# Optimization experiments

Hardware: AMD Instinct MI355X
Metric: run time of the kernel (lower is better)

The kernel has to match this reference:

```python
import jax, jax.numpy as jnp
import numpy as np

N, E = 100000, 1600000
IN_C, OUT_C, H, EDGE_DIM = 128, 64, 2, 4
NEG_SLOPE = 0.2
LN_EPS = 1e-5


def setup_inputs() -> dict:
    key = jax.random.key(0)
    ks = jax.random.split(key, 12)
    s = 1.0 / np.sqrt(IN_C)
    inp = {
        "x": jax.random.normal(ks[0], (N, IN_C), jnp.float32),
        "edge_index": jax.random.randint(ks[1], (2, E), 0, N, jnp.int64),
        "edge_attr": jax.random.normal(ks[2], (E, EDGE_DIM), jnp.float32),
        "W": jax.random.normal(ks[3], (IN_C, H * OUT_C), jnp.float32) * s,
        "att_src": jax.random.normal(ks[4], (H, OUT_C), jnp.float32) * s,
        "att_dst": jax.random.normal(ks[5], (H, OUT_C), jnp.float32) * s,
        "W_edge": jax.random.normal(ks[6], (EDGE_DIM, H * OUT_C), jnp.float32) * 0.5,
        "att_edge": jax.random.normal(ks[7], (H, OUT_C), jnp.float32) * s,
        "bias": jnp.zeros((OUT_C,), jnp.float32),
        "gamma": jnp.ones((OUT_C,), jnp.float32),
        "beta": jnp.zeros((OUT_C,), jnp.float32),
    }
    return inp


def reference(x, edge_index, edge_attr, W, att_src, att_dst, W_edge, att_edge, bias, gamma, beta):
    n = x.shape[0]
    src, dst = edge_index[0], edge_index[1]
    # shared src/dst linear (PyG GATConv with single input tensor)
    h = (x @ W).reshape(n, H, OUT_C)                       # [N,H,C]
    a_src = jnp.einsum("nhc,hc->nh", h, att_src)          # [N,H]
    a_dst = jnp.einsum("nhc,hc->nh", h, att_dst)          # [N,H]
    e = (edge_attr @ W_edge).reshape(-1, H, OUT_C)         # [E,H,C]
    a_edge = jnp.einsum("ehc,hc->eh", e, att_edge)        # [E,H]
    alpha = jax.nn.leaky_relu(a_src[src] + a_dst[dst] + a_edge, NEG_SLOPE)  # [E,H]
    # segment softmax over edges grouped by destination node
    amax = jax.ops.segment_max(alpha, dst, num_segments=n)
    ex = jnp.exp(alpha - amax[dst])
    denom = jax.ops.segment_sum(ex, dst, num_segments=n)
    w = ex / (denom[dst] + 1e-16)                          # [E,H]
    msg = h[src] * w[:, :, None]                           # [E,H,C]
    out = jax.ops.segment_sum(msg, dst, num_segments=n)    # [N,H,C]
    out = out.mean(axis=1) + bias                          # concat=False -> head mean
    # LayerNorm + ReLU
    mu = out.mean(-1, keepdims=True)
    var = ((out - mu) ** 2).mean(-1, keepdims=True)
    out = (out - mu) * jax.lax.rsqrt(var + LN_EPS) * gamma + beta
    return jax.nn.relu(out)
```

## Files before the change

### kernel.cpp

```cpp
#include <hip/hip_runtime.h>
#include <hip/hip_fp16.h>
#include <math.h>

#define IN_C 128
#define HC   128
#define OUT_C 64
#define NEG_SLOPE 0.2f
#define LN_EPS 1e-5f
#define CHUNK 4096
#define NBMAX 1024

typedef __attribute__((ext_vector_type(8))) short bf16x8;
typedef __attribute__((ext_vector_type(4))) float f32x4;

__device__ inline unsigned bf16pack(float a, float b) {
    unsigned ua = __float_as_uint(a), ub = __float_as_uint(b);
    ua = (ua + 0x7fffu + ((ua >> 16) & 1u)) >> 16;
    ub = (ub + 0x7fffu + ((ub >> 16) & 1u)) >> 16;
    return ua | (ub << 16);
}

__global__ __launch_bounds__(256) void k_pre(const float* __restrict__ W,
                                             const float* __restrict__ W_edge,
                                             const float* __restrict__ att_edge,
                                             const int* __restrict__ ei_dst,
                                             unsigned short* __restrict__ WbfT,
                                             float* __restrict__ V,
                                             int* __restrict__ off,
                                             int E, int NB, int PB) {
    __shared__ int hist[NBMAX];
    int b = blockIdx.x, t = threadIdx.x;
    if (b < 8) {
        #pragma unroll
        for (int i = 0; i < 8; ++i) {
            int idx = b * 2048 + i * 256 + t;
            int k = idx >> 7, col = idx & 127;
            unsigned u = __float_as_uint(W[idx]);
            WbfT[col * 128 + k] =
                (unsigned short)((u + 0x7fffu + ((u >> 16) & 1u)) >> 16);
        }
        return;
    }
    if (b == 8) {
        if (t < 8) {
            int d = t >> 1, h = t & 1;
            float s = 0.f;
            for (int c = 0; c < 64; ++c)
                s += W_edge[d * HC + h * 64 + c] * att_edge[h * 64 + c];
            V[d * 2 + h] = s;
        }
        return;
    }
    int pb = b - 9;
    for (int i = t; i < NB; i += 256) hist[i] = 0;
    __syncthreads();
    int base = pb * CHUNK;
    int lim = E - base; if (lim > CHUNK) lim = CHUNK;
    for (int i = t; i < lim; i += 256)
        atomicAdd(&hist[ei_dst[base + i] >> 7], 1);
    __syncthreads();
    for (int i = t; i < NB; i += 256)
        off[(size_t)i * PB + pb] = hist[i];
}

__global__ __launch_bounds__(256) void k_mid(const float* __restrict__ x,
                                             const unsigned short* __restrict__ WbfT,
                                             const float* __restrict__ attS,
                                             const float* __restrict__ attD,
                                             unsigned* __restrict__ hb,
                                             float* __restrict__ a_src,
                                             float* __restrict__ a_dst, int M,
                                             int* __restrict__ off,
                                             int* __restrict__ bsum,
                                             int nS, int GB) {
    __shared__ unsigned xb[64 * 64];
    const int t = threadIdx.x;
    const int bid = blockIdx.x;

    if (bid >= GB) {
        int* sm = (int*)xb;
        int blk = bid - GB;
        int base = blk * 1024 + t * 4;
        int v0 = 0, v1 = 0, v2 = 0, v3 = 0;
        if (base + 0 < nS) v0 = off[base + 0];
        if (base + 1 < nS) v1 = off[base + 1];
        if (base + 2 < nS) v2 = off[base + 2];
        if (base + 3 < nS) v3 = off[base + 3];
        int s = v0 + v1 + v2 + v3;
        sm[t] = s;
        __syncthreads();
        for (int o = 1; o < 256; o <<= 1) {
            int u = (t >= o) ? sm[t - o] : 0;
            __syncthreads();
            sm[t] += u;
            __syncthreads();
        }
        int excl = sm[t] - s;
        if (base + 0 < nS) off[base + 0] = excl;
        if (base + 1 < nS) off[base + 1] = excl + v0;
        if (base + 2 < nS) off[base + 2] = excl + v0 + v1;
        if (base + 3 < nS) off[base + 3] = excl + v0 + v1 + v2;
        if (t == 255) bsum[blk] = sm[255];
        return;
    }

    const int brow = bid * 64;
    const float4* x4 = (const float4*)x;
    #pragma unroll
    for (int i = 0; i < 8; ++i) {
        int idx = i * 256 + t;
        int row = idx >> 5, c4 = idx & 31;
        float4 v = make_float4(0.f, 0.f, 0.f, 0.f);
        if (brow + row < M) v = x4[(size_t)(brow + row) * 32 + c4];
        unsigned lo = bf16pack(v.x, v.y), hi = bf16pack(v.z, v.w);
        int byte = row * 256 + ((c4 * 8) ^ ((row & 7) << 4));
        *(uint2*)((char*)xb + byte) = make_uint2(lo, hi);
    }
    __syncthreads();

    const int w = t >> 6, lane = t & 63;
    const int col = lane & 15, qr = lane >> 4;
    f32x4 acc[8];
    #pragma unroll
    for (int ct = 0; ct < 8; ++ct) acc[ct] = (f32x4){0.f, 0.f, 0.f, 0.f};

    const int arow = w * 16 + col;
    #pragma unroll
    for (int ks = 0; ks < 4; ++ks) {
        int abyte = arow * 256 + ((ks * 64 + qr * 16) ^ ((arow & 7) << 4));
        bf16x8 af = *(const bf16x8*)((const char*)xb + abyte);
        #pragma unroll
        for (int ct = 0; ct < 8; ++ct) {
            bf16x8 bfr = *(const bf16x8*)&WbfT[(size_t)(ct * 16 + col) * 128 + ks * 32 + qr * 8];
            acc[ct] = __builtin_amdgcn_mfma_f32_16x16x32_bf16(af, bfr, acc[ct], 0, 0, 0);
        }
    }

    float pS0[4], pS1[4], pD0[4], pD1[4];
    #pragma unroll
    for (int r = 0; r < 4; ++r) { pS0[r] = pS1[r] = pD0[r] = pD1[r] = 0.f; }
    #pragma unroll
    for (int ct = 0; ct < 8; ++ct) {
        float s = attS[ct * 16 + col], d = attD[ct * 16 + col];
        #pragma unroll
        for (int r = 0; r < 4; ++r) {
            float a = acc[ct][r];
            if (ct < 4) { pS0[r] += a * s; pD0[r] += a * d; }
            else        { pS1[r] += a * s; pD1[r] += a * d; }
        }
    }
    #pragma unroll
    for (int m = 1; m < 16; m <<= 1) {
        #pragma unroll
        for (int r = 0; r < 4; ++r) {
            pS0[r] += __shfl_xor(pS0[r], m);
            pS1[r] += __shfl_xor(pS1[r], m);
            pD0[r] += __shfl_xor(pD0[r], m);
            pD1[r] += __shfl_xor(pD1[r], m);
        }
    }
    #pragma unroll
    for (int r = 0; r < 4; ++r) {
        int grow = brow + w * 16 + qr * 4 + r;
        if (grow < M) {
            if (col == 0) {
                a_src[2 * grow + 0] = pS0[r];
                a_src[2 * grow + 1] = pS1[r];
                a_dst[2 * grow + 0] = pD0[r];
                a_dst[2 * grow + 1] = pD1[r];
            }
            #pragma unroll
            for (int ct = 0; ct < 4; ++ct)
                hb[(size_t)grow * 64 + ct * 16 + col] =
                    bf16pack(acc[ct][r], acc[ct + 4][r]);
        }
    }
}

__global__ __launch_bounds__(256) void k_part(const int* __restrict__ ei,
                                              const float* __restrict__ ea,
                                              const float* __restrict__ V,
                                              const int* __restrict__ off,
                                              const int* __restrict__ bsum,
                                              uint2* __restrict__ pA,
                                              int E, int NB, int PB, int nb2) {
    __shared__ int cur[NBMAX];
    __shared__ int bs[512];
    int pb = blockIdx.x, t = threadIdx.x;

    int r0 = (t < nb2) ? bsum[t] : 0;
    int r1 = (t + 256 < nb2) ? bsum[t + 256] : 0;
    bs[t] = r0; bs[t + 256] = r1;
    __syncthreads();
    for (int o = 1; o < 512; o <<= 1) {
        int u0 = (t >= o) ? bs[t - o] : 0;
        int u1 = (t + 256 >= o) ? bs[t + 256 - o] : 0;
        __syncthreads();
        bs[t] += u0; bs[t + 256] += u1;
        __syncthreads();
    }
    bs[t] -= r0; bs[t + 256] -= r1;
    __syncthreads();

    for (int i = t; i < NB; i += 256) {
        size_t oi = (size_t)i * PB + pb;
        cur[i] = off[oi] + bs[(int)(oi >> 10)];
    }
    __syncthreads();
    float v0 = V[0], v1 = V[1], v2 = V[2], v3 = V[3];
    float v4 = V[4], v5 = V[5], v6 = V[6], v7 = V[7];
    int base = pb * CHUNK;
    int lim = E - base; if (lim > CHUNK) lim = CHUNK;
    for (int i = t; i < lim; i += 256) {
        int e = base + i;
        int s = ei[e], d = ei[E + e];
        float4 a = ((const float4*)ea)[e];
        float ae0 = a.x * v0 + a.y * v2 + a.z * v4 + a.w * v6;
        float ae1 = a.x * v1 + a.y * v3 + a.z * v5 + a.w * v7;
        int slot = atomicAdd(&cur[d >> 7], 1);
        __half2 h = __floats2half2_rn(ae0, ae1);
        pA[slot] = make_uint2((unsigned)s | ((unsigned)(d & 127) << 17),
                              *reinterpret_cast<unsigned*>(&h));
    }
}

__global__ __launch_bounds__(256) void k_csr(const uint2* __restrict__ pA,
                                             const int* __restrict__ off,
                                             const int* __restrict__ bsum,
                                             const float* __restrict__ a_src,
                                             const float* __restrict__ a_dst,
                                             int* __restrict__ rowptr,
                                             uint2* __restrict__ payload,
                                             int M, int E, int NB, int PB, int nb2) {
    __shared__ int bs[512];
    __shared__ int cnt[128];
    __shared__ int sc[128];
    __shared__ int cur[128];
    __shared__ float2 adl[128];
    int b = blockIdx.x, t = threadIdx.x;
    int n0 = b << 7;
    int nloc = M - n0; if (nloc > 128) nloc = 128;

    int r0 = (t < nb2) ? bsum[t] : 0;
    int r1 = (t + 256 < nb2) ? bsum[t + 256] : 0;
    bs[t] = r0; bs[t + 256] = r1;
    __syncthreads();
    for (int o = 1; o < 512; o <<= 1) {
        int u0 = (t >= o) ? bs[t - o] : 0;
        int u1 = (t + 256 >= o) ? bs[t + 256 - o] : 0;
        __syncthreads();
        bs[t] += u0; bs[t + 256] += u1;
        __syncthreads();
    }
    bs[t] -= r0; bs[t + 256] -= r1;
    if (t < 128) cnt[t] = 0;
    if (t < 128 && t < nloc) adl[t] = ((const float2*)a_dst)[n0 + t];
    __syncthreads();

    size_t o0 = (size_t)b * PB;
    int s0 = off[o0] + bs[(int)(o0 >> 10)];
    int s1 = E;
    if (b + 1 < NB) {
        size_t o1 = (size_t)(b + 1) * PB;
        s1 = off[o1] + bs[(int)(o1 >> 10)];
    }

    for (int i = s0 + t; i < s1; i += 256)
        atomicAdd(&cnt[(pA[i].x >> 17) & 127], 1);
    __syncthreads();
    if (t < 128) sc[t] = cnt[t];
    __syncthreads();
    for (int o = 1; o < 128; o <<= 1) {
        int u = 0;
        if (t < 128 && t >= o) u = sc[t - o];
        __syncthreads();
        if (t < 128) sc[t] += u;
        __syncthreads();
    }
    if (t < 128) {
        int base = s0 + sc[t] - cnt[t];
        cur[t] = base;
        if (t < nloc) rowptr[n0 + t] = base;
    }
    if (b == NB - 1 && t == 0) rowptr[M] = E;
    __syncthreads();
    for (int i = s0 + t; i < s1; i += 256) {
        uint2 p = pA[i];
        int src = p.x & 0x1FFFF;
        int dl = (p.x >> 17) & 127;
        __half2 aeh = *reinterpret_cast<__half2*>(&p.y);
        float ae0 = __low2float(aeh), ae1 = __high2float(aeh);
        float2 as = ((const float2*)a_src)[src];
        float2 ad = adl[dl];
        float al0 = as.x + ad.x + ae0; al0 = al0 > 0.f ? al0 : NEG_SLOPE * al0;
        float al1 = as.y + ad.y + ae1; al1 = al1 > 0.f ? al1 : NEG_SLOPE * al1;
        __half2 hx = __floats2half2_rn(__expf(al0), __expf(al1));
        int pos = atomicAdd(&cur[dl], 1);
        payload[pos] = make_uint2((unsigned)src, *reinterpret_cast<unsigned*>(&hx));
    }
}

__global__ __launch_bounds__(256) void k_gather(const uint2* __restrict__ payload,
                                                const int* __restrict__ rowptr,
                                                const unsigned* __restrict__ hb,
                                                const float* __restrict__ bias,
                                                const float* __restrict__ gamma,
                                                const float* __restrict__ beta,
                                                float* __restrict__ out, int M) {
    __shared__ uint2 stg[4][64];
    int w = threadIdx.x >> 6, lane = threadIdx.x & 63;
    int n = blockIdx.x * 4 + w;
    if (n >= M) return;
    int beg = rowptr[n], end = rowptr[n + 1];
    float acc0 = 0.f, acc1 = 0.f, pe0 = 0.f, pe1 = 0.f;

    for (int base = beg; base < end; base += 64) {
        int cnt = end - base; if (cnt > 64) cnt = 64;
        uint2 p = make_uint2(0u, 0u);
        if (lane < cnt) p = payload[base + lane];
        stg[w][lane] = p;
        {
            __half2 he = *reinterpret_cast<__half2*>(&p.y);
            pe0 += __low2float(he);
            pe1 += __high2float(he);
        }
        int j = 0;
        for (; j + 4 <= cnt; j += 4) {
            uint2 q0 = stg[w][j + 0], q1 = stg[w][j + 1];
            uint2 q2 = stg[w][j + 2], q3 = stg[w][j + 3];
            int s0 = __builtin_amdgcn_readfirstlane((int)q0.x);
            int s1 = __builtin_amdgcn_readfirstlane((int)q1.x);
            int s2 = __builtin_amdgcn_readfirstlane((int)q2.x);
            int s3 = __builtin_amdgcn_readfirstlane((int)q3.x);
            unsigned h0 = (hb + (size_t)s0 * 64)[lane];
            unsigned h1 = (hb + (size_t)s1 * 64)[lane];
            unsigned h2 = (hb + (size_t)s2 * 64)[lane];
            unsigned h3 = (hb + (size_t)s3 * 64)[lane];
            __half2 e0 = *reinterpret_cast<__half2*>(&q0.y);
            __half2 e1 = *reinterpret_cast<__half2*>(&q1.y);
            __half2 e2 = *reinterpret_cast<__half2*>(&q2.y);
            __half2 e3 = *reinterpret_cast<__half2*>(&q3.y);
            acc0 += __low2float(e0)  * __uint_as_float(h0 << 16);
            acc1 += __high2float(e0) * __uint_as_float(h0 & 0xffff0000u);
            acc0 += __low2float(e1)  * __uint_as_float(h1 << 16);
            acc1 += __high2float(e1) * __uint_as_float(h1 & 0xffff0000u);
            acc0 += __low2float(e2)  * __uint_as_float(h2 << 16);
            acc1 += __high2float(e2) * __uint_as_float(h2 & 0xffff0000u);
            acc0 += __low2float(e3)  * __uint_as_float(h3 << 16);
            acc1 += __high2float(e3) * __uint_as_float(h3 & 0xffff0000u);
        }
        for (; j < cnt; ++j) {
            uint2 q0 = stg[w][j];
            int s0 = __builtin_amdgcn_readfirstlane((int)q0.x);
            unsigned h0 = (hb + (size_t)s0 * 64)[lane];
            __half2 e0 = *reinterpret_cast<__half2*>(&q0.y);
            acc0 += __low2float(e0)  * __uint_as_float(h0 << 16);
            acc1 += __high2float(e0) * __uint_as_float(h0 & 0xffff0000u);
        }
    }

    float d0 = pe0, d1 = pe1;
    #pragma unroll
    for (int m = 32; m; m >>= 1) {
        d0 += __shfl_xor(d0, m);
        d1 += __shfl_xor(d1, m);
    }

    float o = 0.5f * (acc0 / (d0 + 1e-16f) + acc1 / (d1 + 1e-16f)) + bias[lane];
    float mu = o;
    #pragma unroll
    for (int m = 32; m; m >>= 1) mu += __shfl_xor(mu, m);
    mu *= (1.f / 64.f);
    float c = o - mu;
    float v = c * c;
    #pragma unroll
    for (int m = 32; m; m >>= 1) v += __shfl_xor(v, m);
    v *= (1.f / 64.f);
    float y = c * rsqrtf(v + LN_EPS) * gamma[lane] + beta[lane];
    out[(size_t)n * OUT_C + lane] = fmaxf(y, 0.f);
}

extern "C" void kernel_launch(void* const* d_in, const int* in_sizes, int n_in,
                              void* d_out, int out_size, void* d_ws, size_t ws_size,
                              hipStream_t stream) {
    const float* x     = (const float*)d_in[0];
    const int*   ei    = (const int*)d_in[1];
    const float* ea    = (const float*)d_in[2];
    const float* W     = (const float*)d_in[3];
    const float* attS  = (const float*)d_in[4];
    const float* attD  = (const float*)d_in[5];
    const float* We    = (const float*)d_in[6];
    const float* attE  = (const float*)d_in[7];
    const float* bias  = (const float*)d_in[8];
    const float* gamma = (const float*)d_in[9];
    const float* beta  = (const float*)d_in[10];

    const int M  = in_sizes[0] / IN_C;
    const int E  = in_sizes[1] / 2;
    const int NB = (M + 127) >> 7;
    const int PB = (E + CHUNK - 1) / CHUNK;
    const int nS = NB * PB;
    const int nb2 = (nS + 1023) / 1024;
    const int GB = (M + 63) / 64;

    char* ws = (char*)d_ws;
    size_t woff = 0;
    auto alloc = [&](size_t bytes) -> void* {
        void* p = ws + woff;
        woff += (bytes + 255) & ~(size_t)255;
        return p;
    };
    unsigned*       hb     = (unsigned*)      alloc((size_t)M * 64 * 4);
    float*          a_src  = (float*)         alloc((size_t)M * 2 * 4);
    float*          a_dst  = (float*)         alloc((size_t)M * 2 * 4);
    int*            off    = (int*)           alloc((size_t)nS * 4);
    int*            bsum   = (int*)           alloc((size_t)nb2 * 4);
    int*            rowptr = (int*)           alloc((size_t)(M + 1) * 4);
    uint2*          pA     = (uint2*)         alloc((size_t)E * 8);
    uint2*          payload= (uint2*)         alloc((size_t)E * 8);
    unsigned short* WbfT   = (unsigned short*)alloc(128 * 128 * 2);
    float*          V      = (float*)         alloc(32);

    k_pre<<<9 + PB, 256, 0, stream>>>(W, We, attE, ei + E, WbfT, V, off, E, NB, PB);
    k_mid<<<GB + nb2, 256, 0, stream>>>(x, WbfT, attS, attD, hb, a_src, a_dst, M,
                                        off, bsum, nS, GB);
    k_part<<<PB, 256, 0, stream>>>(ei, ea, V, off, bsum, pA, E, NB, PB, nb2);
    k_csr<<<NB, 256, 0, stream>>>(pA, off, bsum, a_src, a_dst, rowptr, payload,
                                  M, E, NB, PB, nb2);
    k_gather<<<(M + 3) / 4, 256, 0, stream>>>(payload, rowptr, hb, bias, gamma, beta,
                                              (float*)d_out, M);
}
```

Measured before the change: 164.4 us.

## Move attention exp into partition kernel and share the block-sum scan

Computes the leaky-ReLU attention logits and their exponentials during edge partitioning instead of in the CSR build. The CSR kernel then only counts and scatters payloads, with no random a_src reads. The partition kernel publishes the scanned block sums once, so the CSR kernel no longer repeats that scan. It also doubles the edge chunk size, vectorizes the histogram loads and adds an 8-way unrolled gather loop. The larger chunk halves the number of partition blocks, which may leave parts of the GPU idle in that phase.

```diff
diff --git a/kernel.cpp b/kernel.cpp
--- a/kernel.cpp
+++ b/kernel.cpp
@@ -7,7 +7,7 @@
 #define OUT_C 64
 #define NEG_SLOPE 0.2f
 #define LN_EPS 1e-5f
-#define CHUNK 4096
+#define CHUNK 8192
 #define NBMAX 1024
 
 typedef __attribute__((ext_vector_type(8))) short bf16x8;
@@ -56,8 +56,19 @@
     __syncthreads();
     int base = pb * CHUNK;
     int lim = E - base; if (lim > CHUNK) lim = CHUNK;
-    for (int i = t; i < lim; i += 256)
-        atomicAdd(&hist[ei_dst[base + i] >> 7], 1);
+    for (int i4 = t; i4 * 4 < lim; i4 += 256) {
+        int idx = base + i4 * 4;
+        if (idx + 3 < base + lim) {
+            int4 v = *(const int4*)&ei_dst[idx];
+            atomicAdd(&hist[v.x >> 7], 1);
+            atomicAdd(&hist[v.y >> 7], 1);
+            atomicAdd(&hist[v.z >> 7], 1);
+            atomicAdd(&hist[v.w >> 7], 1);
+        } else {
+            for (int k = idx; k < base + lim; ++k)
+                atomicAdd(&hist[ei_dst[k] >> 7], 1);
+        }
+    }
     __syncthreads();
     for (int i = t; i < NB; i += 256)
         off[(size_t)i * PB + pb] = hist[i];
@@ -180,27 +191,29 @@
 __global__ __launch_bounds__(256) void k_part(const int* __restrict__ ei,
                                               const float* __restrict__ ea,
                                               const float* __restrict__ V,
+                                              const float* __restrict__ a_src,
+                                              const float* __restrict__ a_dst,
                                               const int* __restrict__ off,
                                               const int* __restrict__ bsum,
+                                              int* __restrict__ bsum2,
                                               uint2* __restrict__ pA,
                                               int E, int NB, int PB, int nb2) {
     __shared__ int cur[NBMAX];
-    __shared__ int bs[512];
+    __shared__ int bs[256];
     int pb = blockIdx.x, t = threadIdx.x;
 
     int r0 = (t < nb2) ? bsum[t] : 0;
-    int r1 = (t + 256 < nb2) ? bsum[t + 256] : 0;
-    bs[t] = r0; bs[t + 256] = r1;
-    __syncthreads();
-    for (int o = 1; o < 512; o <<= 1) {
-        int u0 = (t >= o) ? bs[t - o] : 0;
-        int u1 = (t + 256 >= o) ? bs[t + 256 - o] : 0;
+    bs[t] = r0;
+    __syncthreads();
+    for (int o = 1; o < 256; o <<= 1) {
+        int u = (t >= o) ? bs[t - o] : 0;
         __syncthreads();
-        bs[t] += u0; bs[t + 256] += u1;
+        bs[t] += u;
         __syncthreads();
     }
-    bs[t] -= r0; bs[t + 256] -= r1;
-    __syncthreads();
+    bs[t] -= r0;
+    __syncthreads();
+    if (pb == 0 && t < nb2) bsum2[t] = bs[t];
 
     for (int i = t; i < NB; i += 256) {
         size_t oi = (size_t)i * PB + pb;
@@ -211,59 +224,46 @@
     float v4 = V[4], v5 = V[5], v6 = V[6], v7 = V[7];
     int base = pb * CHUNK;
     int lim = E - base; if (lim > CHUNK) lim = CHUNK;
+    #pragma unroll 2
     for (int i = t; i < lim; i += 256) {
         int e = base + i;
         int s = ei[e], d = ei[E + e];
         float4 a = ((const float4*)ea)[e];
         float ae0 = a.x * v0 + a.y * v2 + a.z * v4 + a.w * v6;
         float ae1 = a.x * v1 + a.y * v3 + a.z * v5 + a.w * v7;
+        float2 as = ((const float2*)a_src)[s];
+        float2 ad = ((const float2*)a_dst)[d];
+        float al0 = as.x + ad.x + ae0; al0 = al0 > 0.f ? al0 : NEG_SLOPE * al0;
+        float al1 = as.y + ad.y + ae1; al1 = al1 > 0.f ? al1 : NEG_SLOPE * al1;
+        __half2 hx = __floats2half2_rn(__expf(al0), __expf(al1));
         int slot = atomicAdd(&cur[d >> 7], 1);
-        __half2 h = __floats2half2_rn(ae0, ae1);
         pA[slot] = make_uint2((unsigned)s | ((unsigned)(d & 127) << 17),
-                              *reinterpret_cast<unsigned*>(&h));
+                              *reinterpret_cast<unsigned*>(&hx));
     }
 }
 
 __global__ __launch_bounds__(256) void k_csr(const uint2* __restrict__ pA,
                                              const int* __restrict__ off,
-                                             const int* __restrict__ bsum,
-                                             const float* __restrict__ a_src,
-                                             const float* __restrict__ a_dst,
+                                             const int* __restrict__ bsum2,
                                              int* __restrict__ rowptr,
                                              uint2* __restrict__ payload,
-                                             int M, int E, int NB, int PB, int nb2) {
-    __shared__ int bs[512];
+                                             int M, int E, int NB, int PB) {
     __shared__ int cnt[128];
     __shared__ int sc[128];
     __shared__ int cur[128];
-    __shared__ float2 adl[128];
     int b = blockIdx.x, t = threadIdx.x;
     int n0 = b << 7;
     int nloc = M - n0; if (nloc > 128) nloc = 128;
 
-    int r0 = (t < nb2) ? bsum[t] : 0;
-    int r1 = (t + 256 < nb2) ? bsum[t + 256] : 0;
-    bs[t] = r0; bs[t + 256] = r1;
-    __syncthreads();
-    for (int o = 1; o < 512; o <<= 1) {
-        int u0 = (t >= o) ? bs[t - o] : 0;
-        int u1 = (t + 256 >= o) ? bs[t + 256 - o] : 0;
-        __syncthreads();
-        bs[t] += u0; bs[t + 256] += u1;
-        __syncthreads();
-    }
-    bs[t] -= r0; bs[t + 256] -= r1;
-    if (t < 128) cnt[t] = 0;
-    if (t < 128 && t < nloc) adl[t] = ((const float2*)a_dst)[n0 + t];
-    __syncthreads();
-
     size_t o0 = (size_t)b * PB;
-    int s0 = off[o0] + bs[(int)(o0 >> 10)];
+    int s0 = off[o0] + bsum2[(int)(o0 >> 10)];
     int s1 = E;
     if (b + 1 < NB) {
         size_t o1 = (size_t)(b + 1) * PB;
-        s1 = off[o1] + bs[(int)(o1 >> 10)];
-    }
+        s1 = off[o1] + bsum2[(int)(o1 >> 10)];
+    }
+    if (t < 128) cnt[t] = 0;
+    __syncthreads();
 
     for (int i = s0 + t; i < s1; i += 256)
         atomicAdd(&cnt[(pA[i].x >> 17) & 127], 1);
@@ -286,17 +286,9 @@
     __syncthreads();
     for (int i = s0 + t; i < s1; i += 256) {
         uint2 p = pA[i];
-        int src = p.x & 0x1FFFF;
         int dl = (p.x >> 17) & 127;
-        __half2 aeh = *reinterpret_cast<__half2*>(&p.y);
-        float ae0 = __low2float(aeh), ae1 = __high2float(aeh);
-        float2 as = ((const float2*)a_src)[src];
-        float2 ad = adl[dl];
-        float al0 = as.x + ad.x + ae0; al0 = al0 > 0.f ? al0 : NEG_SLOPE * al0;
-        float al1 = as.y + ad.y + ae1; al1 = al1 > 0.f ? al1 : NEG_SLOPE * al1;
-        __half2 hx = __floats2half2_rn(__expf(al0), __expf(al1));
         int pos = atomicAdd(&cur[dl], 1);
-        payload[pos] = make_uint2((unsigned)src, *reinterpret_cast<unsigned*>(&hx));
+        payload[pos] = make_uint2(p.x & 0x1FFFF, p.y);
     }
 }
 
@@ -325,6 +317,52 @@
             pe1 += __high2float(he);
         }
         int j = 0;
+        for (; j + 8 <= cnt; j += 8) {
+            uint2 q0 = stg[w][j + 0], q1 = stg[w][j + 1];
+            uint2 q2 = stg[w][j + 2], q3 = stg[w][j + 3];
+            uint2 q4 = stg[w][j + 4], q5 = stg[w][j + 5];
+            uint2 q6 = stg[w][j + 6], q7 = stg[w][j + 7];
+            int s0 = __builtin_amdgcn_readfirstlane((int)q0.x);
+            int s1 = __builtin_amdgcn_readfirstlane((int)q1.x);
+            int s2 = __builtin_amdgcn_readfirstlane((int)q2.x);
+            int s3 = __builtin_amdgcn_readfirstlane((int)q3.x);
+            int s4 = __builtin_amdgcn_readfirstlane((int)q4.x);
+            int s5 = __builtin_amdgcn_readfirstlane((int)q5.x);
+            int s6 = __builtin_amdgcn_readfirstlane((int)q6.x);
+            int s7 = __builtin_amdgcn_readfirstlane((int)q7.x);
+            unsigned h0 = (hb + (size_t)s0 * 64)[lane];
+            unsigned h1 = (hb + (size_t)s1 * 64)[lane];
+            unsigned h2 = (hb + (size_t)s2 * 64)[lane];
+            unsigned h3 = (hb + (size_t)s3 * 64)[lane];
+            unsigned h4 = (hb + (size_t)s4 * 64)[lane];
+            unsigned h5 = (hb + (size_t)s5 * 64)[lane];
+            unsigned h6 = (hb + (size_t)s6 * 64)[lane];
+            unsigned h7 = (hb + (size_t)s7 * 64)[lane];
+            __half2 e0 = *reinterpret_cast<__half2*>(&q0.y);
+            __half2 e1 = *reinterpret_cast<__half2*>(&q1.y);
+            __half2 e2 = *reinterpret_cast<__half2*>(&q2.y);
+            __half2 e3 = *reinterpret_cast<__half2*>(&q3.y);
+            __half2 e4 = *reinterpret_cast<__half2*>(&q4.y);
+            __half2 e5 = *reinterpret_cast<__half2*>(&q5.y);
+            __half2 e6 = *reinterpret_cast<__half2*>(&q6.y);
+            __half2 e7 = *reinterpret_cast<__half2*>(&q7.y);
+            acc0 += __low2float(e0)  * __uint_as_float(h0 << 16);
+            acc1 += __high2float(e0) * __uint_as_float(h0 & 0xffff0000u);
+            acc0 += __low2float(e1)  * __uint_as_float(h1 << 16);
+            acc1 += __high2float(e1) * __uint_as_float(h1 & 0xffff0000u);
+            acc0 += __low2float(e2)  * __uint_as_float(h2 << 16);
+            acc1 += __high2float(e2) * __uint_as_float(h2 & 0xffff0000u);
+            acc0 += __low2float(e3)  * __uint_as_float(h3 << 16);
+            acc1 += __high2float(e3) * __uint_as_float(h3 & 0xffff0000u);
+            acc0 += __low2float(e4)  * __uint_as_float(h4 << 16);
+            acc1 += __high2float(e4) * __uint_as_float(h4 & 0xffff0000u);
+            acc0 += __low2float(e5)  * __uint_as_float(h5 << 16);
+            acc1 += __high2float(e5) * __uint_as_float(h5 & 0xffff0000u);
+            acc0 += __low2float(e6)  * __uint_as_float(h6 << 16);
+            acc1 += __high2float(e6) * __uint_as_float(h6 & 0xffff0000u);
+            acc0 += __low2float(e7)  * __uint_as_float(h7 << 16);
+            acc1 += __high2float(e7) * __uint_as_float(h7 & 0xffff0000u);
+        }
         for (; j + 4 <= cnt; j += 4) {
             uint2 q0 = stg[w][j + 0], q1 = stg[w][j + 1];
             uint2 q2 = stg[w][j + 2], q3 = stg[w][j + 3];
@@ -415,6 +453,7 @@
     float*          a_dst  = (float*)         alloc((size_t)M * 2 * 4);
     int*            off    = (int*)           alloc((size_t)nS * 4);
     int*            bsum   = (int*)           alloc((size_t)nb2 * 4);
+    int*            bsum2  = (int*)           alloc((size_t)nb2 * 4);
     int*            rowptr = (int*)           alloc((size_t)(M + 1) * 4);
     uint2*          pA     = (uint2*)         alloc((size_t)E * 8);
     uint2*          payload= (uint2*)         alloc((size_t)E * 8);
@@ -424,9 +463,9 @@
     k_pre<<<9 + PB, 256, 0, stream>>>(W, We, attE, ei + E, WbfT, V, off, E, NB, PB);
     k_mid<<<GB + nb2, 256, 0, stream>>>(x, WbfT, attS, attD, hb, a_src, a_dst, M,
                                         off, bsum, nS, GB);
-    k_part<<<PB, 256, 0, stream>>>(ei, ea, V, off, bsum, pA, E, NB, PB, nb2);
-    k_csr<<<NB, 256, 0, stream>>>(pA, off, bsum, a_src, a_dst, rowptr, payload,
-                                  M, E, NB, PB, nb2);
+    k_part<<<PB, 256, 0, stream>>>(ei, ea, V, a_src, a_dst, off, bsum, bsum2,
+                                   pA, E, NB, PB, nb2);
+    k_csr<<<NB, 256, 0, stream>>>(pA, off, bsum2, rowptr, payload, M, E, NB, PB);
     k_gather<<<(M + 3) / 4, 256, 0, stream>>>(payload, rowptr, hb, bias, gamma, beta,
                                               (float*)d_out, M);
 }
```

Measured after the change: 161.8 us. No clear change (-1.6%).
